# Kernel optimization log

Measured on AMD Instinct MI355X. Metric: run time of the kernel, lower is better.

The kernel has to match this reference:

```python
import jax, jax.numpy as jnp
import numpy as np

EMB = 512
HEADS = 8

def setup_inputs() -> dict:
    key = jax.random.key(0)
    ks = jax.random.split(key, 9)
    s = 1.0 / np.sqrt(EMB)
    return {
        'x':  jax.random.normal(ks[0], (4, 2048, EMB), dtype=jnp.float32),
        'Wq': jax.random.uniform(ks[1], (EMB, EMB), jnp.float32, -s, s),
        'bq': jax.random.uniform(ks[2], (EMB,), jnp.float32, -s, s),
        'Wk': jax.random.uniform(ks[3], (EMB, EMB), jnp.float32, -s, s),
        'bk': jax.random.uniform(ks[4], (EMB,), jnp.float32, -s, s),
        'Wv': jax.random.uniform(ks[5], (EMB, EMB), jnp.float32, -s, s),
        'bv': jax.random.uniform(ks[6], (EMB,), jnp.float32, -s, s),
        'Wo': jax.random.uniform(ks[7], (EMB, EMB), jnp.float32, -s, s),
        'bo': jax.random.uniform(ks[8], (EMB,), jnp.float32, -s, s),
    }

def reference(x, Wq, bq, Wk, bk, Wv, bv, Wo, bo):
    b, n, e = x.shape
    h = HEADS
    d = e // h
    def split_heads(t):
        return t.reshape(b, n, h, d).transpose(0, 2, 1, 3)  # b h n d
    q = split_heads(x @ Wq.T + bq)
    k = split_heads(x @ Wk.T + bk)
    v = split_heads(x @ Wv.T + bv)
    energy = jnp.einsum('bhqd,bhkd->bhqk', q, k)
    scaling = jnp.sqrt(jnp.float32(e))  # NOTE: sqrt(emb_size), not sqrt(head_dim), per source
    att = jax.nn.softmax(energy / scaling, axis=-1)
    out = jnp.einsum('bhal,bhlv->bhav', att, v)  # b h n d
    out = out.transpose(0, 2, 1, 3).reshape(b, n, e)
    return out @ Wo.T + bo
```

## Files before the change

### kernel.cpp

```cpp
#include <hip/hip_runtime.h>

typedef float f32x4 __attribute__((ext_vector_type(4)));
typedef float f32x16 __attribute__((ext_vector_type(16)));
typedef short bf16x8 __attribute__((ext_vector_type(8)));
typedef unsigned int uint;
typedef unsigned short ushort_t;

#define EMB    512
#define NSEQ   2048
#define NBATCH 4
#define NHEAD  8
#define MROWS  (NBATCH * NSEQ)
#define CEXP   0.06375872f

__device__ __forceinline__ uint f2bf(float x) {
    uint u = __builtin_bit_cast(uint, x);
    return (u + 0x7fffu + ((u >> 16) & 1u)) >> 16;
}

__device__ __forceinline__ void glds16(const void* g, void* l) {
    __builtin_amdgcn_global_load_lds(
        (const __attribute__((address_space(1))) uint*)g,
        (__attribute__((address_space(3))) uint*)l, 16, 0, 0);
}

__global__ __launch_bounds__(256)
void prep(const float* __restrict__ x,
          const float* __restrict__ Wq, const float* __restrict__ Wk,
          const float* __restrict__ Wv, const float* __restrict__ Wo,
          const float* __restrict__ bq, const float* __restrict__ bk,
          const float* __restrict__ bv,
          ushort_t* __restrict__ xb, ushort_t* __restrict__ Wqkvb,
          float* __restrict__ bqkv, ushort_t* __restrict__ Wob) {
    int t = blockIdx.x * 256 + threadIdx.x;
    {
        float4 v = ((const float4*)x)[t];
        uint2 p;
        p.x = f2bf(v.x) | (f2bf(v.y) << 16);
        p.y = f2bf(v.z) | (f2bf(v.w) << 16);
        ((uint2*)xb)[t] = p;
    }
    if (t < 65536) {
        float4 a = ((const float4*)Wq)[t];
        float4 b = ((const float4*)Wk)[t];
        float4 c = ((const float4*)Wv)[t];
        float4 d = ((const float4*)Wo)[t];
        uint2 p;
        p.x = f2bf(a.x) | (f2bf(a.y) << 16); p.y = f2bf(a.z) | (f2bf(a.w) << 16);
        ((uint2*)Wqkvb)[t] = p;
        p.x = f2bf(b.x) | (f2bf(b.y) << 16); p.y = f2bf(b.z) | (f2bf(b.w) << 16);
        ((uint2*)Wqkvb)[t + 65536] = p;
        p.x = f2bf(c.x) | (f2bf(c.y) << 16); p.y = f2bf(c.z) | (f2bf(c.w) << 16);
        ((uint2*)Wqkvb)[t + 131072] = p;
        p.x = f2bf(d.x) | (f2bf(d.y) << 16); p.y = f2bf(d.z) | (f2bf(d.w) << 16);
        ((uint2*)Wob)[t] = p;
    }
    if (t < 512) {
        bqkv[t] = bq[t]; bqkv[512 + t] = bk[t]; bqkv[1024 + t] = bv[t];
    }
}

template<int MODE>
__global__ __launch_bounds__(256)
void gemm64(const ushort_t* __restrict__ A, const ushort_t* __restrict__ BT,
            const float* __restrict__ bias, ushort_t* __restrict__ oQK,
            ushort_t* __restrict__ oVT, float* __restrict__ oC) {
    __shared__ __align__(16) char smem[32768];
    ushort_t (*As)[2][64][32] = (ushort_t (*)[2][64][32])smem;
    ushort_t (*Bs)[2][64][32] = (ushort_t (*)[2][64][32])(smem + 16384);
    float (*ep)[68] = (float (*)[68])smem;
    float (*epV)[69] = (float (*)[69])smem;

    const int tid = threadIdx.x, wave = tid >> 6, lane = tid & 63;
    const int m0 = blockIdx.x * 64, n0 = blockIdx.y * 64;
    const int wr = (wave & 1) * 32, wc = (wave >> 1) * 32;

    f32x4 acc[2][2];
#pragma unroll
    for (int i = 0; i < 2; ++i)
#pragma unroll
        for (int j = 0; j < 2; ++j) acc[i][j] = (f32x4){0.f, 0.f, 0.f, 0.f};

    const int grow = wave * 16 + (lane >> 2);
    const int gcol = (lane & 3) * 8;
    const ushort_t* Ag = A  + (size_t)(m0 + grow) * 512 + gcol;
    const ushort_t* Bg = BT + (size_t)(n0 + grow) * 512 + gcol;
    const int fr = lane & 15, fc = (lane >> 4) * 8;

#pragma unroll
    for (int t = 0; t < 2; ++t) {
        glds16(Ag + t * 32, &As[0][t][wave * 16][0]);
        glds16(Bg + t * 32, &Bs[0][t][wave * 16][0]);
    }
    __syncthreads();

    int p = 0;
    for (int kt = 0; kt < 8; ++kt) {
        if (kt < 7) {
#pragma unroll
            for (int t = 0; t < 2; ++t) {
                glds16(Ag + (kt + 1) * 64 + t * 32, &As[p ^ 1][t][wave * 16][0]);
                glds16(Bg + (kt + 1) * 64 + t * 32, &Bs[p ^ 1][t][wave * 16][0]);
            }
        }
#pragma unroll
        for (int t = 0; t < 2; ++t) {
            bf16x8 af[2], bf[2];
#pragma unroll
            for (int i = 0; i < 2; ++i) af[i] = *(const bf16x8*)&As[p][t][wr + i * 16 + fr][fc];
#pragma unroll
            for (int j = 0; j < 2; ++j) bf[j] = *(const bf16x8*)&Bs[p][t][wc + j * 16 + fr][fc];
#pragma unroll
            for (int i = 0; i < 2; ++i)
#pragma unroll
                for (int j = 0; j < 2; ++j)
                    acc[i][j] = __builtin_amdgcn_mfma_f32_16x16x32_bf16(af[i], bf[j], acc[i][j], 0, 0, 0);
        }
        __syncthreads();
        p ^= 1;
    }

    const int col_l = lane & 15, row_l = (lane >> 4) * 4;

    if (MODE == 0 && n0 >= 1024) {
        const int e0 = n0 - 1024;
#pragma unroll
        for (int j = 0; j < 2; ++j) {
            const float bvv = bias[n0 + wc + j * 16 + col_l];
#pragma unroll
            for (int i = 0; i < 2; ++i) {
                f32x4 v = acc[i][j];
#pragma unroll
                for (int r = 0; r < 4; ++r)
                    epV[wc + j * 16 + col_l][wr + i * 16 + row_l + r] = v[r] + bvv;
            }
        }
        __syncthreads();
        const int e = tid >> 2, ts = (tid & 3) * 16;
        const int bb = m0 >> 11, tok = (m0 & 2047) + ts;
        uint o[8];
#pragma unroll
        for (int k = 0; k < 8; ++k)
            o[k] = f2bf(epV[e][ts + 2 * k]) | (f2bf(epV[e][ts + 2 * k + 1]) << 16);
        ushort_t* dst = &oVT[((size_t)(bb * 512 + e0 + e)) * 2048 + tok];
        *(uint4*)dst       = *(const uint4*)&o[0];
        *(uint4*)(dst + 8) = *(const uint4*)&o[4];
        return;
    }

    const float scale = (MODE == 0 && n0 < 512) ? CEXP : 1.0f;
    float bv[2];
#pragma unroll
    for (int j = 0; j < 2; ++j) bv[j] = bias[n0 + wc + j * 16 + col_l];

    const int erow = tid >> 3, eseg = (tid & 7) * 8;
#pragma unroll
    for (int c = 0; c < 2; ++c) {
        __syncthreads();
        if (wr == c * 32) {
#pragma unroll
            for (int i = 0; i < 2; ++i) {
#pragma unroll
                for (int j = 0; j < 2; ++j) {
                    f32x4 v = acc[i][j];
#pragma unroll
                    for (int r = 0; r < 4; ++r)
                        ep[i * 16 + row_l + r][wc + j * 16 + col_l] = (v[r] + bv[j]) * scale;
                }
            }
        }
        __syncthreads();
        const int grow2 = m0 + c * 32 + erow;
        if (MODE == 0) {
            uint4 o0;
#pragma unroll
            for (int k = 0; k < 4; ++k) {
                ((uint*)&o0)[k] = f2bf(ep[erow][eseg + k * 2])
                                | (f2bf(ep[erow][eseg + k * 2 + 1]) << 16);
            }
            *(uint4*)&oQK[(size_t)grow2 * 1024 + n0 + eseg] = o0;
        } else {
#pragma unroll
            for (int k = 0; k < 2; ++k) {
                f32x4 v = *(const f32x4*)&ep[erow][eseg + k * 4];
                *(f32x4*)&oC[(size_t)grow2 * 512 + n0 + eseg + k * 4] = v;
            }
        }
    }
}

template<int NSLICE>
__global__ __launch_bounds__(256, 2)
void attn_mfma(const ushort_t* __restrict__ QK, const ushort_t* __restrict__ VT,
               ushort_t* __restrict__ Op, float* __restrict__ Lp,
               ushort_t* __restrict__ AO) {
    __shared__ ushort_t Ks[2][64][72];
    __shared__ ushort_t Vs[2][64][72];

    const int tid = threadIdx.x, w = tid >> 6, lane = tid & 63;
    int qt, bh, slice;
    if (NSLICE == 2) {
        const int wgid = blockIdx.x;
        const int g = (wgid & 7) | ((wgid >> 6) << 3);
        qt = (wgid >> 3) & 7;
        bh = g & 31;
        slice = g >> 5;
    } else {
        qt = blockIdx.x; bh = blockIdx.y; slice = 0;
    }
    const int b = bh >> 3, h = bh & 7;
    const int l31 = lane & 31, lhi = lane >> 5;

    const int tok0 = qt * 256 + w * 64 + l31;
    bf16x8 qf[2][4];
#pragma unroll
    for (int g = 0; g < 2; ++g)
#pragma unroll
        for (int ks = 0; ks < 4; ++ks)
            qf[g][ks] = *(const bf16x8*)&QK[(size_t)(b * NSEQ + tok0 + g * 32) * 1024
                                            + h * 64 + ks * 16 + lhi * 8];

    f32x16 accO[2][2];
    f32x16 accL[2];
#pragma unroll
    for (int g = 0; g < 2; ++g) {
#pragma unroll
        for (int i = 0; i < 16; ++i) { accO[g][0][i] = 0.f; accO[g][1][i] = 0.f; accL[g][i] = 0.f; }
    }
    union { uint u[4]; bf16x8 v; } ONE;
    ONE.u[0] = 0x3f803f80u; ONE.u[1] = 0x3f803f80u;
    ONE.u[2] = 0x3f803f80u; ONE.u[3] = 0x3f803f80u;

    const int sr = tid & 63, sc = (tid >> 6) * 16;
    const ushort_t* Kg = QK + (size_t)(b * NSEQ) * 1024 + 512 + h * 64;
    const ushort_t* Vg = VT + ((size_t)(b * 512 + h * 64)) * 2048;

    const int kt0 = slice * (32 / NSLICE), kt1 = kt0 + 32 / NSLICE;

    {
        const int k0 = kt0 * 64;
        uint4 kv0 = *(const uint4*)&Kg[(size_t)(k0 + sr) * 1024 + sc];
        uint4 kv1 = *(const uint4*)&Kg[(size_t)(k0 + sr) * 1024 + sc + 8];
        uint4 vv0 = *(const uint4*)&Vg[(size_t)sr * 2048 + k0 + sc];
        uint4 vv1 = *(const uint4*)&Vg[(size_t)sr * 2048 + k0 + sc + 8];
        *(uint4*)&Ks[0][sr][sc] = kv0;  *(uint4*)&Ks[0][sr][sc + 8] = kv1;
        *(uint4*)&Vs[0][sr][sc] = vv0;  *(uint4*)&Vs[0][sr][sc + 8] = vv1;
        __syncthreads();
    }

    const uint psel = 0x07060302u;
    int p = 0;
#pragma unroll 2
    for (int kt = kt0; kt < kt1; ++kt) {
        uint4 kv0, kv1, vv0, vv1;
        const bool pf = (kt + 1 < kt1);
        if (pf) {
            const int k0 = (kt + 1) * 64;
            kv0 = *(const uint4*)&Kg[(size_t)(k0 + sr) * 1024 + sc];
            kv1 = *(const uint4*)&Kg[(size_t)(k0 + sr) * 1024 + sc + 8];
            vv0 = *(const uint4*)&Vg[(size_t)sr * 2048 + k0 + sc];
            vv1 = *(const uint4*)&Vg[(size_t)sr * 2048 + k0 + sc + 8];
        }

#pragma unroll
        for (int ms = 0; ms < 2; ++ms) {
            bf16x8 ka[4];
#pragma unroll
            for (int ks = 0; ks < 4; ++ks)
                ka[ks] = *(const bf16x8*)&Ks[p][ms * 32 + l31][ks * 16 + lhi * 8];

            f32x16 st[2];
#pragma unroll
            for (int g = 0; g < 2; ++g)
#pragma unroll
                for (int i = 0; i < 16; ++i) st[g][i] = 0.f;
            __builtin_amdgcn_s_setprio(1);
#pragma unroll
            for (int ks = 0; ks < 4; ++ks) {
                st[0] = __builtin_amdgcn_mfma_f32_32x32x16_bf16(ka[ks], qf[0][ks], st[0], 0, 0, 0);
                st[1] = __builtin_amdgcn_mfma_f32_32x32x16_bf16(ka[ks], qf[1][ks], st[1], 0, 0, 0);
            }
            __builtin_amdgcn_s_setprio(0);

            uint dd[2][8];
#pragma unroll
            for (int g = 0; g < 2; ++g)
#pragma unroll
                for (int i = 0; i < 8; ++i) {
                    uint ua = __builtin_bit_cast(uint, __builtin_amdgcn_exp2f(st[g][2 * i]));
                    uint ub = __builtin_bit_cast(uint, __builtin_amdgcn_exp2f(st[g][2 * i + 1]));
                    uint r;
                    asm("v_perm_b32 %0, %1, %2, %3" : "=v"(r) : "v"(ub), "v"(ua), "v"(psel));
                    dd[g][i] = r;
                }

#pragma unroll
            for (int s = 0; s < 2; ++s) {
                const int step = ms * 2 + s;
                bf16x8 va0 = *(const bf16x8*)&Vs[p][l31][step * 16 + lhi * 8];
                bf16x8 va1 = *(const bf16x8*)&Vs[p][32 + l31][step * 16 + lhi * 8];
#pragma unroll
                for (int g = 0; g < 2; ++g) {
                    uint a0 = dd[g][4 * s + 0], a2 = dd[g][4 * s + 2];
                    uint a1 = dd[g][4 * s + 1], a3 = dd[g][4 * s + 3];
                    asm("v_permlane32_swap_b32 %0, %1" : "+v"(a0), "+v"(a2));
                    asm("v_permlane32_swap_b32 %0, %1" : "+v"(a1), "+v"(a3));
                    union { uint u[4]; bf16x8 v; } B;
                    B.u[0] = a0; B.u[1] = a1; B.u[2] = a2; B.u[3] = a3;
                    __builtin_amdgcn_s_setprio(1);
                    accO[g][0] = __builtin_amdgcn_mfma_f32_32x32x16_bf16(va0, B.v, accO[g][0], 0, 0, 0);
                    accO[g][1] = __builtin_amdgcn_mfma_f32_32x32x16_bf16(va1, B.v, accO[g][1], 0, 0, 0);
                    accL[g]    = __builtin_amdgcn_mfma_f32_32x32x16_bf16(ONE.v, B.v, accL[g], 0, 0, 0);
                    __builtin_amdgcn_s_setprio(0);
                }
            }
        }

        if (pf) {
            *(uint4*)&Ks[p ^ 1][sr][sc] = kv0;  *(uint4*)&Ks[p ^ 1][sr][sc + 8] = kv1;
            *(uint4*)&Vs[p ^ 1][sr][sc] = vv0;  *(uint4*)&Vs[p ^ 1][sr][sc + 8] = vv1;
        }
        __syncthreads();
        p ^= 1;
    }

    if (NSLICE == 1) {
#pragma unroll
        for (int g = 0; g < 2; ++g) {
            const float inv = 1.0f / accL[g][0];
#pragma unroll
            for (int hf = 0; hf < 2; ++hf)
#pragma unroll
                for (int r = 0; r < 16; ++r) {
                    const int d = (r & 3) + 8 * (r >> 2) + 4 * lhi + 32 * hf;
                    AO[((size_t)(b * NSEQ + tok0 + g * 32)) * 512 + h * 64 + d] =
                        (ushort_t)f2bf(accO[g][hf][r] * inv);
                }
        }
    } else {
        if (lane < 32) {
#pragma unroll
            for (int g = 0; g < 2; ++g)
                Lp[(size_t)slice * 65536 + bh * 2048 + tok0 + g * 32] = accL[g][0];
        }
        ushort_t* Os = Op + (size_t)slice * 4194304;
#pragma unroll
        for (int g = 0; g < 2; ++g)
#pragma unroll
            for (int hf = 0; hf < 2; ++hf)
#pragma unroll
                for (int r = 0; r < 16; ++r) {
                    const int d = (r & 3) + 8 * (r >> 2) + 4 * lhi + 32 * hf;
                    Os[((size_t)(bh * 64 + d)) * 2048 + tok0 + g * 32] =
                        (ushort_t)f2bf(accO[g][hf][r]);
                }
    }
}

__global__ __launch_bounds__(256)
void combine2Tb(const ushort_t* __restrict__ Op, const float* __restrict__ Lp,
                ushort_t* __restrict__ AO) {
    __shared__ float T[64][68];
    const int tid = threadIdx.x;
    const int tc = blockIdx.x, bh = blockIdx.y;
    const int b = bh >> 3, h = bh & 7;
    const int tok0 = tc * 64;

    const int d = tid >> 2, ts = (tid & 3) * 16;
    float acc[16];
#pragma unroll
    for (int i = 0; i < 16; ++i) acc[i] = 0.f;
#pragma unroll
    for (int s = 0; s < 2; ++s) {
        const ushort_t* P = Op + (size_t)s * 4194304
                               + ((size_t)(bh * 64 + d)) * 2048 + tok0 + ts;
#pragma unroll
        for (int k2 = 0; k2 < 2; ++k2) {
            uint4 u = *(const uint4*)(P + 8 * k2);
#pragma unroll
            for (int j = 0; j < 4; ++j) {
                uint uw = ((const uint*)&u)[j];
                acc[k2 * 8 + 2 * j]     += __builtin_bit_cast(float, uw << 16);
                acc[k2 * 8 + 2 * j + 1] += __builtin_bit_cast(float, uw & 0xffff0000u);
            }
        }
    }
#pragma unroll
    for (int k = 0; k < 4; ++k)
        *(f32x4*)&T[d][ts + 4 * k] = *(const f32x4*)&acc[4 * k];
    __syncthreads();

    const int tk = tid >> 2, ds = (tid & 3) * 16;
    const int tok = tok0 + tk;
    const float inv = 1.0f / (Lp[bh * 2048 + tok] + Lp[65536 + bh * 2048 + tok]);
    uint o[8];
#pragma unroll
    for (int k = 0; k < 8; ++k) {
        float a = T[ds + 2 * k][tk] * inv;
        float c = T[ds + 2 * k + 1][tk] * inv;
        o[k] = f2bf(a) | (f2bf(c) << 16);
    }
    ushort_t* dst = AO + ((size_t)(b * NSEQ + tok)) * 512 + h * 64 + ds;
    *(uint4*)dst       = *(const uint4*)&o[0];
    *(uint4*)(dst + 8) = *(const uint4*)&o[4];
}

extern "C" void kernel_launch(void* const* d_in, const int* in_sizes, int n_in,
                              void* d_out, int out_size, void* d_ws, size_t ws_size,
                              hipStream_t stream) {
    const float* x  = (const float*)d_in[0];
    const float* Wq = (const float*)d_in[1];
    const float* bq = (const float*)d_in[2];
    const float* Wk = (const float*)d_in[3];
    const float* bk = (const float*)d_in[4];
    const float* Wv = (const float*)d_in[5];
    const float* bv = (const float*)d_in[6];
    const float* Wo = (const float*)d_in[7];
    const float* bo = (const float*)d_in[8];

    char* ws = (char*)d_ws;
    ushort_t* xb    = (ushort_t*)(ws);
    ushort_t* Wqkvb = (ushort_t*)(ws + 8388608);
    ushort_t* Wob   = (ushort_t*)(ws + 9961472);
    float*    bqkv  = (float*)   (ws + 10485760);
    ushort_t* QKb   = (ushort_t*)(ws + 10491904);
    ushort_t* VTg   = (ushort_t*)(ws + 27269120);
    ushort_t* AOb   = (ushort_t*)(ws + 35657728);
    ushort_t* Opart = (ushort_t*)(ws + 44046336);
    float*    Lpart = (float*)   (ws);
    const bool split = ws_size >= 78125056;

    prep<<<4096, 256, 0, stream>>>(x, Wq, Wk, Wv, Wo, bq, bk, bv,
                                   xb, Wqkvb, bqkv, Wob);
    gemm64<0><<<dim3(128, 24), 256, 0, stream>>>(xb, Wqkvb, bqkv, QKb, VTg, nullptr);
    if (split) {
        attn_mfma<2><<<dim3(512), 256, 0, stream>>>(QKb, VTg, Opart, Lpart, nullptr);
        combine2Tb<<<dim3(32, 32), 256, 0, stream>>>(Opart, Lpart, AOb);
    } else {
        attn_mfma<1><<<dim3(8, 32), 256, 0, stream>>>(QKb, VTg, nullptr, nullptr, AOb);
    }
    gemm64<1><<<dim3(128, 8), 256, 0, stream>>>(AOb, Wob, bo, nullptr, nullptr, (float*)d_out);
}
```

Baseline: 164.9 us.

## Use 128x128 tiles for QKV projection GEMM, split out output GEMM kernel

New measurement: 177.6 us. 1.08x slower.

```diff
diff --git a/kernel.cpp b/kernel.cpp
--- a/kernel.cpp
+++ b/kernel.cpp
@@ -60,26 +60,25 @@
     }
 }
 
-template<int MODE>
 __global__ __launch_bounds__(256)
-void gemm64(const ushort_t* __restrict__ A, const ushort_t* __restrict__ BT,
-            const float* __restrict__ bias, ushort_t* __restrict__ oQK,
-            ushort_t* __restrict__ oVT, float* __restrict__ oC) {
+void gemmQKV(const ushort_t* __restrict__ A, const ushort_t* __restrict__ BT,
+             const float* __restrict__ bias, ushort_t* __restrict__ oQK,
+             ushort_t* __restrict__ oVT) {
     __shared__ __align__(16) char smem[32768];
-    ushort_t (*As)[2][64][32] = (ushort_t (*)[2][64][32])smem;
-    ushort_t (*Bs)[2][64][32] = (ushort_t (*)[2][64][32])(smem + 16384);
-    float (*ep)[68] = (float (*)[68])smem;
+    ushort_t (*As)[128][32] = (ushort_t (*)[128][32])smem;
+    ushort_t (*Bs)[128][32] = (ushort_t (*)[128][32])(smem + 16384);
+    float (*ep)[132] = (float (*)[132])smem;
     float (*epV)[69] = (float (*)[69])smem;
 
     const int tid = threadIdx.x, wave = tid >> 6, lane = tid & 63;
-    const int m0 = blockIdx.x * 64, n0 = blockIdx.y * 64;
-    const int wr = (wave & 1) * 32, wc = (wave >> 1) * 32;
-
-    f32x4 acc[2][2];
-#pragma unroll
-    for (int i = 0; i < 2; ++i)
-#pragma unroll
-        for (int j = 0; j < 2; ++j) acc[i][j] = (f32x4){0.f, 0.f, 0.f, 0.f};
+    const int m0 = blockIdx.x * 128, n0 = blockIdx.y * 128;
+    const int wr = (wave & 1) * 64, wc = (wave >> 1) * 64;
+
+    f32x4 acc[4][4];
+#pragma unroll
+    for (int i = 0; i < 4; ++i)
+#pragma unroll
+        for (int j = 0; j < 4; ++j) acc[i][j] = (f32x4){0.f, 0.f, 0.f, 0.f};
 
     const int grow = wave * 16 + (lane >> 2);
     const int gcol = (lane & 3) * 8;
@@ -87,6 +86,127 @@
     const ushort_t* Bg = BT + (size_t)(n0 + grow) * 512 + gcol;
     const int fr = lane & 15, fc = (lane >> 4) * 8;
 
+    for (int kt = 0; kt < 8; ++kt) {
+        __syncthreads();
+#pragma unroll
+        for (int t = 0; t < 2; ++t) {
+            glds16(Ag + kt * 64 + t * 32,            &As[t][wave * 16][0]);
+            glds16(Ag + kt * 64 + t * 32 + 64 * 512, &As[t][64 + wave * 16][0]);
+            glds16(Bg + kt * 64 + t * 32,            &Bs[t][wave * 16][0]);
+            glds16(Bg + kt * 64 + t * 32 + 64 * 512, &Bs[t][64 + wave * 16][0]);
+        }
+        __syncthreads();
+#pragma unroll
+        for (int t = 0; t < 2; ++t) {
+            bf16x8 af[4], bf[4];
+#pragma unroll
+            for (int i = 0; i < 4; ++i) af[i] = *(const bf16x8*)&As[t][wr + i * 16 + fr][fc];
+#pragma unroll
+            for (int j = 0; j < 4; ++j) bf[j] = *(const bf16x8*)&Bs[t][wc + j * 16 + fr][fc];
+#pragma unroll
+            for (int i = 0; i < 4; ++i)
+#pragma unroll
+                for (int j = 0; j < 4; ++j)
+                    acc[i][j] = __builtin_amdgcn_mfma_f32_16x16x32_bf16(af[i], bf[j], acc[i][j], 0, 0, 0);
+        }
+    }
+
+    const int col_l = lane & 15, row_l = (lane >> 4) * 4;
+
+    if (n0 >= 1024) {
+        const int e0 = n0 - 1024;
+        const int bb = m0 >> 11, tokb = m0 & 2047;
+#pragma unroll
+        for (int q = 0; q < 4; ++q) {
+            const int eh = q >> 1, th = q & 1;
+            __syncthreads();
+            if (wr == th * 64 && wc == eh * 64) {
+#pragma unroll
+                for (int j = 0; j < 4; ++j) {
+                    const float bvv = bias[n0 + wc + j * 16 + col_l];
+#pragma unroll
+                    for (int i = 0; i < 4; ++i) {
+                        f32x4 v = acc[i][j];
+#pragma unroll
+                        for (int r = 0; r < 4; ++r)
+                            epV[j * 16 + col_l][i * 16 + row_l + r] = v[r] + bvv;
+                    }
+                }
+            }
+            __syncthreads();
+            const int e = tid >> 2, ts = (tid & 3) * 16;
+            uint o[8];
+#pragma unroll
+            for (int k = 0; k < 8; ++k)
+                o[k] = f2bf(epV[e][ts + 2 * k]) | (f2bf(epV[e][ts + 2 * k + 1]) << 16);
+            ushort_t* dst = &oVT[((size_t)(bb * 512 + e0 + eh * 64 + e)) * 2048
+                                 + tokb + th * 64 + ts];
+            *(uint4*)dst       = *(const uint4*)&o[0];
+            *(uint4*)(dst + 8) = *(const uint4*)&o[4];
+        }
+        return;
+    }
+
+    const float scale = (n0 < 512) ? CEXP : 1.0f;
+    float bv[4];
+#pragma unroll
+    for (int j = 0; j < 4; ++j) bv[j] = bias[n0 + wc + j * 16 + col_l];
+
+    const int erow = tid >> 3, eseg = (tid & 7) * 16;
+#pragma unroll
+    for (int c = 0; c < 4; ++c) {
+        __syncthreads();
+        if (wr == (c >> 1) * 64) {
+#pragma unroll
+            for (int ii = 0; ii < 2; ++ii) {
+                const int i = (c & 1) * 2 + ii;
+#pragma unroll
+                for (int j = 0; j < 4; ++j) {
+                    f32x4 v = acc[i][j];
+#pragma unroll
+                    for (int r = 0; r < 4; ++r)
+                        ep[ii * 16 + row_l + r][wc + j * 16 + col_l] = (v[r] + bv[j]) * scale;
+                }
+            }
+        }
+        __syncthreads();
+        const int grow2 = m0 + c * 32 + erow;
+        uint4 o0, o1;
+#pragma unroll
+        for (int k = 0; k < 4; ++k) {
+            uint lo = f2bf(ep[erow][eseg + k * 2])     | (f2bf(ep[erow][eseg + k * 2 + 1]) << 16);
+            uint hi = f2bf(ep[erow][eseg + 8 + k * 2]) | (f2bf(ep[erow][eseg + 9 + k * 2]) << 16);
+            ((uint*)&o0)[k] = lo; ((uint*)&o1)[k] = hi;
+        }
+        *(uint4*)&oQK[(size_t)grow2 * 1024 + n0 + eseg]     = o0;
+        *(uint4*)&oQK[(size_t)grow2 * 1024 + n0 + eseg + 8] = o1;
+    }
+}
+
+__global__ __launch_bounds__(256)
+void gemmOut64(const ushort_t* __restrict__ A, const ushort_t* __restrict__ BT,
+               const float* __restrict__ bias, float* __restrict__ oC) {
+    __shared__ __align__(16) char smem[32768];
+    ushort_t (*As)[2][64][32] = (ushort_t (*)[2][64][32])smem;
+    ushort_t (*Bs)[2][64][32] = (ushort_t (*)[2][64][32])(smem + 16384);
+    float (*ep)[68] = (float (*)[68])smem;
+
+    const int tid = threadIdx.x, wave = tid >> 6, lane = tid & 63;
+    const int m0 = blockIdx.x * 64, n0 = blockIdx.y * 64;
+    const int wr = (wave & 1) * 32, wc = (wave >> 1) * 32;
+
+    f32x4 acc[2][2];
+#pragma unroll
+    for (int i = 0; i < 2; ++i)
+#pragma unroll
+        for (int j = 0; j < 2; ++j) acc[i][j] = (f32x4){0.f, 0.f, 0.f, 0.f};
+
+    const int grow = wave * 16 + (lane >> 2);
+    const int gcol = (lane & 3) * 8;
+    const ushort_t* Ag = A  + (size_t)(m0 + grow) * 512 + gcol;
+    const ushort_t* Bg = BT + (size_t)(n0 + grow) * 512 + gcol;
+    const int fr = lane & 15, fc = (lane >> 4) * 8;
+
 #pragma unroll
     for (int t = 0; t < 2; ++t) {
         glds16(Ag + t * 32, &As[0][t][wave * 16][0]);
@@ -121,34 +241,6 @@
     }
 
     const int col_l = lane & 15, row_l = (lane >> 4) * 4;
-
-    if (MODE == 0 && n0 >= 1024) {
-        const int e0 = n0 - 1024;
-#pragma unroll
-        for (int j = 0; j < 2; ++j) {
-            const float bvv = bias[n0 + wc + j * 16 + col_l];
-#pragma unroll
-            for (int i = 0; i < 2; ++i) {
-                f32x4 v = acc[i][j];
-#pragma unroll
-                for (int r = 0; r < 4; ++r)
-                    epV[wc + j * 16 + col_l][wr + i * 16 + row_l + r] = v[r] + bvv;
-            }
-        }
-        __syncthreads();
-        const int e = tid >> 2, ts = (tid & 3) * 16;
-        const int bb = m0 >> 11, tok = (m0 & 2047) + ts;
-        uint o[8];
-#pragma unroll
-        for (int k = 0; k < 8; ++k)
-            o[k] = f2bf(epV[e][ts + 2 * k]) | (f2bf(epV[e][ts + 2 * k + 1]) << 16);
-        ushort_t* dst = &oVT[((size_t)(bb * 512 + e0 + e)) * 2048 + tok];
-        *(uint4*)dst       = *(const uint4*)&o[0];
-        *(uint4*)(dst + 8) = *(const uint4*)&o[4];
-        return;
-    }
-
-    const float scale = (MODE == 0 && n0 < 512) ? CEXP : 1.0f;
     float bv[2];
 #pragma unroll
     for (int j = 0; j < 2; ++j) bv[j] = bias[n0 + wc + j * 16 + col_l];
@@ -165,26 +257,16 @@
                     f32x4 v = acc[i][j];
 #pragma unroll
                     for (int r = 0; r < 4; ++r)
-                        ep[i * 16 + row_l + r][wc + j * 16 + col_l] = (v[r] + bv[j]) * scale;
+                        ep[i * 16 + row_l + r][wc + j * 16 + col_l] = v[r] + bv[j];
                 }
             }
         }
         __syncthreads();
         const int grow2 = m0 + c * 32 + erow;
-        if (MODE == 0) {
-            uint4 o0;
-#pragma unroll
-            for (int k = 0; k < 4; ++k) {
-                ((uint*)&o0)[k] = f2bf(ep[erow][eseg + k * 2])
-                                | (f2bf(ep[erow][eseg + k * 2 + 1]) << 16);
-            }
-            *(uint4*)&oQK[(size_t)grow2 * 1024 + n0 + eseg] = o0;
-        } else {
-#pragma unroll
-            for (int k = 0; k < 2; ++k) {
-                f32x4 v = *(const f32x4*)&ep[erow][eseg + k * 4];
-                *(f32x4*)&oC[(size_t)grow2 * 512 + n0 + eseg + k * 4] = v;
-            }
+#pragma unroll
+        for (int k = 0; k < 2; ++k) {
+            f32x4 v = *(const f32x4*)&ep[erow][eseg + k * 4];
+            *(f32x4*)&oC[(size_t)grow2 * 512 + n0 + eseg + k * 4] = v;
         }
     }
 }
@@ -432,12 +514,12 @@
 
     prep<<<4096, 256, 0, stream>>>(x, Wq, Wk, Wv, Wo, bq, bk, bv,
                                    xb, Wqkvb, bqkv, Wob);
-    gemm64<0><<<dim3(128, 24), 256, 0, stream>>>(xb, Wqkvb, bqkv, QKb, VTg, nullptr);
+    gemmQKV<<<dim3(64, 12), 256, 0, stream>>>(xb, Wqkvb, bqkv, QKb, VTg);
     if (split) {
         attn_mfma<2><<<dim3(512), 256, 0, stream>>>(QKb, VTg, Opart, Lpart, nullptr);
         combine2Tb<<<dim3(32, 32), 256, 0, stream>>>(Opart, Lpart, AOb);
     } else {
         attn_mfma<1><<<dim3(8, 32), 256, 0, stream>>>(QKb, VTg, nullptr, nullptr, AOb);
     }
-    gemm64<1><<<dim3(128, 8), 256, 0, stream>>>(AOb, Wob, bo, nullptr, nullptr, (float*)d_out);
-}
+    gemmOut64<<<dim3(128, 8), 256, 0, stream>>>(AOb, Wob, bo, (float*)d_out);
+}
```
